# Kernel optimization log

Measured on AMD Instinct MI355X. Metric: run time of the kernel, lower is better.

## Reference

```python
import jax, jax.numpy as jnp
import numpy as np

PD = 3                      # spatial feature dim (z, y, x)
HB = 1024                   # hash base per lattice coordinate
HOFF = 512                  # offset: lattice coords assumed in [-512, 511]
FILL = np.int32(2**31 - 1)  # sentinel for padded hash slots
EPS = 2.220446049250313e-16 # np.finfo('float').eps as in the torch module

def _elev_mat():
    # Embedding onto hyperplane sum(x)=0 with std-dev scale factors
    # (canonical permutohedral-lattice elevation, Adams et al.).
    E = np.zeros((PD + 1, PD), np.float32)
    E[0] = 1.0
    for i in range(1, PD + 1):
        E[i, i - 1] = -i
        E[i, i:] = 1.0
    inv_std = np.sqrt(2.0 / 3.0) * (PD + 1)
    scale = inv_std / np.sqrt(np.arange(1, PD + 1) * np.arange(2, PD + 2))
    return (E * scale[None, :]).astype(np.float32)

_EMAT = _elev_mat()
_IU = np.triu(np.ones((PD + 1, PD + 1), bool), 1)   # j > i
_IL = np.tril(np.ones((PD + 1, PD + 1), bool), -1)  # j < i

def _hash(k):  # (..., PD) int32 -> (...,) int32, injective for |coord| < 512
    return ((k[..., 0] + HOFF) * HB + (k[..., 1] + HOFF)) * HB + (k[..., 2] + HOFF)

def permutohedral(values, features):
    """Splat-blur-slice Gaussian filter. values (N,VD), features (N,PD)."""
    N, VD = values.shape
    elevated = features @ jnp.asarray(_EMAT).T                  # (N, PD+1)
    # nearest remainder-0 lattice point (nearest multiple of PD+1, ties -> down)
    v = elevated / (PD + 1)
    up, down = jnp.ceil(v), jnp.floor(v)
    rem0 = jnp.where(up - v < v - down, up, down) * (PD + 1)
    diff = elevated - rem0
    lt = diff[:, :, None] < diff[:, None, :]
    le = diff[:, :, None] <= diff[:, None, :]
    rank = (lt & _IU).sum(-1) + (le & _IL).sum(-1)              # (N, PD+1) int32
    rank = rank + jnp.round(rem0.sum(-1) / (PD + 1)).astype(rank.dtype)[:, None]
    shift = jnp.where(rank < 0, PD + 1, 0) + jnp.where(rank > PD, -(PD + 1), 0)
    rank = rank + shift
    rem0 = rem0 + shift.astype(rem0.dtype)
    # barycentric coordinates inside the enclosing simplex
    t = (elevated - rem0) / (PD + 1)                            # (N, PD+1)
    ohA = jax.nn.one_hot(PD - rank, PD + 2, dtype=values.dtype)
    ohB = jax.nn.one_hot(PD + 1 - rank, PD + 2, dtype=values.dtype)
    b = (ohA * t[..., None]).sum(1) - (ohB * t[..., None]).sum(1)
    b = b.at[:, 0].add(1.0 + b[:, PD + 1])
    bary = b[:, :PD + 1]                                        # (N, PD+1)
    # keys of the PD+1 simplex vertices (first PD coords; last is implied)
    rem0i = rem0[:, :PD].astype(jnp.int32)
    ranki = rank[:, :PD].astype(jnp.int32)
    r = jnp.arange(PD + 1, dtype=jnp.int32)[None, :, None]
    keys = rem0i[:, None, :] + jnp.where(ranki[:, None, :] >= PD + 1 - r, r - (PD + 1), r)  # (N,PD+1,PD)
    h = _hash(keys).reshape(-1)                                 # (N*(PD+1),)
    M = h.shape[0]
    uh, inv = jnp.unique(h, size=M, fill_value=FILL, return_inverse=True)
    inv = inv.reshape(-1)
    # splat
    contrib = (values[:, None, :] * bary[:, :, None]).reshape(M, VD)
    lat = jax.ops.segment_sum(contrib, inv, num_segments=M)     # (M, VD)
    # decode unique keys from the (invertible) hash
    k2 = uh % HB - HOFF
    tq = uh // HB
    k1 = tq % HB - HOFF
    k0 = tq // HB - HOFF
    ukeys = jnp.stack([k0, k1, k2], -1).astype(jnp.int32)       # (M, PD)
    valid = (uh != FILL)[:, None]
    # blur with [0.5, 1, 0.5] along each of the PD+1 lattice directions
    def lookup(nk, lat_):
        nh = _hash(nk)
        idx = jnp.clip(jnp.searchsorted(uh, nh), 0, M - 1)
        ok = (uh[idx] == nh)[:, None]
        return jnp.where(ok, lat_[idx], 0.0)
    for j in range(PD + 1):
        o = np.ones(PD, np.int32)
        if j < PD:
            o[j] = -PD
        o = jnp.asarray(o)
        lat = jnp.where(valid, lat + 0.5 * (lookup(ukeys + o, lat) + lookup(ukeys - o, lat)), 0.0)
    # slice
    alpha = 1.0 / (1.0 + 2.0 ** (-PD))
    return alpha * jnp.einsum('nr,nrv->nv', bary, lat[inv.reshape(-1, PD + 1)])

def spatial_features(image, v_gamma, sigma_gamma):
    _, d, h, w = image.shape
    z = jnp.arange(d, dtype=jnp.float32)[:, None, None]
    y = jnp.arange(h, dtype=jnp.float32)[None, :, None]
    x = jnp.arange(w, dtype=jnp.float32)[None, None, :]
    zz = v_gamma[0] * jnp.broadcast_to(z, (d, h, w)) / sigma_gamma[0]
    xx = v_gamma[1] * jnp.broadcast_to(x, (d, h, w)) / sigma_gamma[1]
    yy = v_gamma[2] * jnp.broadcast_to(y, (d, h, w)) / sigma_gamma[2]
    return jnp.stack([zz, yy, xx], axis=3)                      # (d,h,w,3)

def setup_inputs() -> dict:
    key = jax.random.key(0)
    k1, k2 = jax.random.split(key)
    C, D, H, W = 4, 64, 128, 128
    return {
        'input_': jax.random.normal(k1, (C, D, H, W), jnp.float32),
        'image': jax.random.normal(k2, (1, D, H, W), jnp.float32),
        'v_gamma': jnp.ones((3,), jnp.float32),       # nn.Parameter init [1,1,1]
        'sigma_gamma': 5.0 * jnp.ones((3,), jnp.float32),
    }

def reference(input_, image, v_gamma, sigma_gamma):
    C, d, h, w = input_.shape
    N = d * h * w
    feats = spatial_features(image, v_gamma, sigma_gamma).reshape(N, PD)
    # filter q and the all-ones normalizer in one pass (linear per channel)
    vals = jnp.concatenate([input_.reshape(C, N).T, jnp.ones((N, 1), jnp.float32)], axis=1)
    out = permutohedral(vals, feats)
    q = out[:, :C].T.reshape(C, d, h, w)
    norm = out[:, C].reshape(1, d, h, w)
    return q * (1.0 / (norm + EPS))
```

## Files before the change

### kernel.cpp

```cpp
#include <hip/hip_runtime.h>


#define DD    64
#define HHH   128
#define WWW   128
#define NPTS  (DD * HHH * WWW)
#define LATN  (1 << 17)
#define SH_BITS 10
#define SHSZ (1 << SH_BITS)

__device__ __forceinline__ int encK(int K0, int K1, int K2) {
    return ((K2 >> 2) << 12) | ((K1 >> 2) << 7) | ((K0 >> 2) << 2) | (K0 & 3);
}

__device__ __forceinline__ void pl_geom(int z, int y, int x,
                                        const float* __restrict__ vg,
                                        const float* __restrict__ sg,
                                        int* didx, float* bout) {
    float f0 = vg[0] * (float)z / sg[0];
    float f1 = vg[2] * (float)y / sg[2];
    float f2 = vg[1] * (float)x / sg[1];

    const float m00 = (float)2.3094010767585034;
    const float m01 = (float)1.3333333333333333;
    const float m02 = (float)0.9428090415820634;
    const float m21 = (float)-2.6666666666666665;
    const float m32 = (float)-2.8284271247461903;

    float e[4];
    e[0] =  m00 * f0 + m01 * f1 + m02 * f2;
    e[1] = -m00 * f0 + m01 * f1 + m02 * f2;
    e[2] =  m21 * f1 + m02 * f2;
    e[3] =  m32 * f2;

    float rem0[4];
    int sumr = 0;
    #pragma unroll
    for (int i = 0; i < 4; ++i) {
        float v = e[i] * 0.25f;
        float up = ceilf(v), dn = floorf(v);
        float rr = ((up - v) < (v - dn)) ? up : dn;
        rem0[i] = rr * 4.0f;
        sumr += (int)rem0[i];
    }
    sumr /= 4;

    float diff[4];
    #pragma unroll
    for (int i = 0; i < 4; ++i) diff[i] = e[i] - rem0[i];
    int rank[4] = {0, 0, 0, 0};
    #pragma unroll
    for (int i = 0; i < 4; ++i)
        #pragma unroll
        for (int j = i + 1; j < 4; ++j) {
            if (diff[i] < diff[j]) rank[i]++; else rank[j]++;
        }

    #pragma unroll
    for (int i = 0; i < 4; ++i) {
        rank[i] += sumr;
        if (rank[i] < 0)      { rank[i] += 4; rem0[i] += 4.0f; }
        else if (rank[i] > 3) { rank[i] -= 4; rem0[i] -= 4.0f; }
    }

    float b[5] = {0.f, 0.f, 0.f, 0.f, 0.f};
    #pragma unroll
    for (int i = 0; i < 4; ++i) {
        float t = (e[i] - rem0[i]) * 0.25f;
        b[3 - rank[i]] += t;
        b[4 - rank[i]] -= t;
    }
    b[0] += 1.0f + b[4];

    int k0 = (int)rem0[0], k1 = (int)rem0[1], k2 = (int)rem0[2];
    #pragma unroll
    for (int r = 0; r < 4; ++r) {
        int o0 = (rank[0] >= 4 - r) ? (r - 4) : r;
        int o1 = (rank[1] >= 4 - r) ? (r - 4) : r;
        int o2 = (rank[2] >= 4 - r) ? (r - 4) : r;
        int K0 = (k0 + o0 + 16) & 127;
        int K1 = (k1 + o1 + 48) & 127;
        int K2 = (k2 + o2 + 88) & 127;
        didx[r] = encK(K0, K1, K2);
        bout[r] = b[r];
    }
}

__device__ __forceinline__ void pl_emit(int key, const float* a,
                                        int* skey, float (*sacc)[5],
                                        float* __restrict__ lat,
                                        unsigned char* __restrict__ exists) {
    unsigned idx = ((unsigned)key * 2654435761u) >> (32 - SH_BITS);
    int probes = 0;
    bool inlds = true;
    for (;;) {
        int cur = skey[idx];
        if (cur == key) break;
        if (cur == -1) {
            cur = atomicCAS(&skey[idx], -1, key);
            if (cur == -1 || cur == key) break;
        }
        idx = (idx + 1) & (SHSZ - 1);
        if (++probes >= SHSZ) { inlds = false; break; }
    }
    if (inlds) {
        #pragma unroll
        for (int c = 0; c < 5; ++c) atomicAdd(&sacc[idx][c], a[c]);
    } else {
        float* L = lat + (size_t)key * 5;
        #pragma unroll
        for (int c = 0; c < 5; ++c) atomicAdd(L + c, a[c]);
        exists[key] = 1;
    }
}

__global__ __launch_bounds__(512, 6)
void pl_splat(const float* __restrict__ vals, const float* __restrict__ vg,
              const float* __restrict__ sg, float* __restrict__ lat,
              unsigned char* __restrict__ exists) {
    __shared__ int   skey[SHSZ];
    __shared__ float sacc[SHSZ][5];
    for (int i = threadIdx.x; i < SHSZ; i += 512) {
        skey[i] = -1;
        #pragma unroll
        for (int c = 0; c < 5; ++c) sacc[i][c] = 0.f;
    }
    __syncthreads();

    int bt = blockIdx.x;
    int lx = threadIdx.x & 15;
    int ly = (threadIdx.x >> 4) & 7;
    int lz = threadIdx.x >> 7;
    int x0 = ((bt & 3) << 5) + (lx << 1);
    int y  = (((bt >> 2) & 15) << 3) + ly;
    int z  = ((bt >> 6) << 2) + lz;
    int n0 = (z << 14) + (y << 7) + x0;

    float2 c0 = *(const float2*)(vals + n0);
    float2 c1 = *(const float2*)(vals + NPTS + n0);
    float2 c2 = *(const float2*)(vals + 2 * NPTS + n0);
    float2 c3 = *(const float2*)(vals + 3 * NPTS + n0);

    int ckey[4];
    float acc[4][5];
    {
        int didx[4]; float b[4];
        pl_geom(z, y, x0, vg, sg, didx, b);
        #pragma unroll
        for (int r = 0; r < 4; ++r) {
            ckey[r] = didx[r];
            float w = b[r];
            acc[r][0] = w * c0.x; acc[r][1] = w * c1.x;
            acc[r][2] = w * c2.x; acc[r][3] = w * c3.x;
            acc[r][4] = w;
        }
    }
    {
        int didx[4]; float b[4];
        pl_geom(z, y, x0 + 1, vg, sg, didx, b);
        #pragma unroll
        for (int r = 0; r < 4; ++r) {
            float w = b[r];
            if (didx[r] == ckey[r]) {
                acc[r][0] += w * c0.y; acc[r][1] += w * c1.y;
                acc[r][2] += w * c2.y; acc[r][3] += w * c3.y;
                acc[r][4] += w;
            } else {
                pl_emit(ckey[r], acc[r], skey, sacc, lat, exists);
                ckey[r] = didx[r];
                acc[r][0] = w * c0.y; acc[r][1] = w * c1.y;
                acc[r][2] = w * c2.y; acc[r][3] = w * c3.y;
                acc[r][4] = w;
            }
        }
    }
    #pragma unroll
    for (int r = 0; r < 4; ++r)
        pl_emit(ckey[r], acc[r], skey, sacc, lat, exists);

    __syncthreads();

    int rot = (blockIdx.x * 131) & (SHSZ - 1);
    for (int ii = threadIdx.x; ii < SHSZ; ii += 512) {
        int i = (ii + rot) & (SHSZ - 1);
        int key = skey[i];
        if (key < 0) continue;
        exists[key] = 1;
        float* L = lat + (size_t)key * 5;
        #pragma unroll
        for (int c = 0; c < 5; ++c) atomicAdd(L + c, sacc[i][c]);
    }
}

__global__ __launch_bounds__(256)
void pl_blur(const float* __restrict__ lin, float* __restrict__ lout,
             const unsigned char* __restrict__ exists,
             int d0, int d1, int d2) {
    int didx = blockIdx.x * 256 + threadIdx.x;
    if (didx >= LATN) return;
    if (!exists[didx]) return;
    int r  = didx & 3;
    int K0 = (((didx >> 2)  & 31) << 2) | r;
    int K1 = (((didx >> 7)  & 31) << 2) | r;
    int K2 = (((didx >> 12) & 31) << 2) | r;
    float acc[5];
    const float* S = lin + (size_t)didx * 5;
    #pragma unroll
    for (int c = 0; c < 5; ++c) acc[c] = S[c];
    #pragma unroll
    for (int sgn = 0; sgn < 2; ++sgn) {
        int a0 = sgn ? -d0 : d0;
        int a1 = sgn ? -d1 : d1;
        int a2 = sgn ? -d2 : d2;
        int P0 = K0 + a0, P1 = K1 + a1, P2 = K2 + a2;
        if (((unsigned)P0 < 128u) & ((unsigned)P1 < 128u) & ((unsigned)P2 < 128u)) {
            const float* L = lin + (size_t)encK(P0, P1, P2) * 5;
            #pragma unroll
            for (int c = 0; c < 5; ++c) acc[c] += 0.5f * L[c];
        }
    }
    float* O = lout + (size_t)didx * 5;
    #pragma unroll
    for (int c = 0; c < 5; ++c) O[c] = acc[c];
}

__global__ __launch_bounds__(256)
void pl_slice(const float* __restrict__ vg, const float* __restrict__ sg,
              const float* __restrict__ lat, float* __restrict__ out) {
    int n = blockIdx.x * 256 + threadIdx.x;
    if (n >= NPTS) return;
    int z = n >> 14;
    int y = (n >> 7) & 127;
    int x = n & 127;
    int didx[4]; float b[4];
    pl_geom(z, y, x, vg, sg, didx, b);
    float a0 = 0.f, a1 = 0.f, a2 = 0.f, a3 = 0.f, a4 = 0.f;
    #pragma unroll
    for (int r = 0; r < 4; ++r) {
        float w = b[r];
        const float* L = lat + (size_t)didx[r] * 5;
        a0 += w * L[0]; a1 += w * L[1]; a2 += w * L[2]; a3 += w * L[3]; a4 += w * L[4];
    }
    const float alpha = (float)(1.0 / 1.125);
    float norm = alpha * a4 + (float)2.220446049250313e-16;
    float invn = 1.0f / norm;
    out[n]            = (alpha * a0) * invn;
    out[NPTS + n]     = (alpha * a1) * invn;
    out[2 * NPTS + n] = (alpha * a2) * invn;
    out[3 * NPTS + n] = (alpha * a3) * invn;
}

extern "C" void kernel_launch(void* const* d_in, const int* in_sizes, int n_in,
                              void* d_out, int out_size, void* d_ws, size_t ws_size,
                              hipStream_t stream) {
    const float* input = (const float*)d_in[0];
    const float* vg = (const float*)d_in[2];
    const float* sg = (const float*)d_in[3];
    float* out = (float*)d_out;

    char* ws = (char*)d_ws;
    size_t off = 0;
    float* lat0 = (float*)(ws + off);            off += (size_t)LATN * 5 * 4;
    float* lat1 = (float*)(ws + off);            off += (size_t)LATN * 5 * 4;
    unsigned char* exists = (unsigned char*)(ws + off); off += LATN;

    hipMemsetAsync(lat0, 0, (size_t)LATN * 5 * 4, stream);
    hipMemsetAsync(lat1, 0, (size_t)LATN * 5 * 4, stream);
    hipMemsetAsync(exists, 0, LATN, stream);

    pl_splat<<<1024, dim3(512), 0, stream>>>(input, vg, sg, lat0, exists);

    const int offs[4][3] = {{-3, 1, 1}, {1, -3, 1}, {1, 1, -3}, {1, 1, 1}};
    float* bufs[2] = {lat0, lat1};
    for (int j = 0; j < 4; ++j) {
        pl_blur<<<LATN / 256, dim3(256), 0, stream>>>(bufs[j & 1], bufs[(j & 1) ^ 1],
                                                      exists,
                                                      offs[j][0], offs[j][1], offs[j][2]);
    }
    pl_slice<<<NPTS / 256, dim3(256), 0, stream>>>(vg, sg, lat0, out);
}
```

Baseline: 186.8 us.

## Fuse blur passes and slice into one persistent kernel with grid barriers

Splat now handles four x-points per thread, so each block covers a larger tile and only half as many blocks launch. Its global atomics are spread across four replicated lattice copies to reduce contention, and those copies are summed inside the first blur pass. The four blur passes and the slice are fused into a single kernel that uses software grid-wide barriers in place of separate launches. Three memsets are merged into one covering a larger region. The grid barrier assumes all 512 blocks are co-resident, which risks deadlock if they are not, and the extra lattice copies increase memset and read traffic.

Result: slower. 537.8 us (+187.9%).

```diff
diff --git a/kernel.cpp b/kernel.cpp
--- a/kernel.cpp
+++ b/kernel.cpp
@@ -6,6 +6,7 @@
 #define WWW   128
 #define NPTS  (DD * HHH * WWW)
 #define LATN  (1 << 17)
+#define LATF  (LATN * 5)
 #define SH_BITS 10
 #define SHSZ (1 << SH_BITS)
 
@@ -88,7 +89,7 @@
 
 __device__ __forceinline__ void pl_emit(int key, const float* a,
                                         int* skey, float (*sacc)[5],
-                                        float* __restrict__ lat,
+                                        float* __restrict__ latc,
                                         unsigned char* __restrict__ exists) {
     unsigned idx = ((unsigned)key * 2654435761u) >> (32 - SH_BITS);
     int probes = 0;
@@ -107,16 +108,16 @@
         #pragma unroll
         for (int c = 0; c < 5; ++c) atomicAdd(&sacc[idx][c], a[c]);
     } else {
-        float* L = lat + (size_t)key * 5;
+        float* L = latc + (size_t)key * 5;
         #pragma unroll
         for (int c = 0; c < 5; ++c) atomicAdd(L + c, a[c]);
         exists[key] = 1;
     }
 }
 
-__global__ __launch_bounds__(512, 6)
+__global__ __launch_bounds__(512, 4)
 void pl_splat(const float* __restrict__ vals, const float* __restrict__ vg,
-              const float* __restrict__ sg, float* __restrict__ lat,
+              const float* __restrict__ sg, float* __restrict__ latc,
               unsigned char* __restrict__ exists) {
     __shared__ int   skey[SHSZ];
     __shared__ float sacc[SHSZ][5];
@@ -127,19 +128,26 @@
     }
     __syncthreads();
 
+    float* mycopy = latc + (size_t)(blockIdx.x & 3) * LATF;
+
     int bt = blockIdx.x;
-    int lx = threadIdx.x & 15;
-    int ly = (threadIdx.x >> 4) & 7;
+    int xs = threadIdx.x & 7;
+    int ly = (threadIdx.x >> 3) & 15;
     int lz = threadIdx.x >> 7;
-    int x0 = ((bt & 3) << 5) + (lx << 1);
-    int y  = (((bt >> 2) & 15) << 3) + ly;
-    int z  = ((bt >> 6) << 2) + lz;
+    int xsl = ((xs & 3) << 1) | (xs >> 2);
+    int x0 = ((bt & 3) << 5) + (xsl << 2);
+    int y  = (((bt >> 2) & 7) << 4) + ly;
+    int z  = ((bt >> 5) << 2) + lz;
     int n0 = (z << 14) + (y << 7) + x0;
 
-    float2 c0 = *(const float2*)(vals + n0);
-    float2 c1 = *(const float2*)(vals + NPTS + n0);
-    float2 c2 = *(const float2*)(vals + 2 * NPTS + n0);
-    float2 c3 = *(const float2*)(vals + 3 * NPTS + n0);
+    float4 q0 = *(const float4*)(vals + n0);
+    float4 q1 = *(const float4*)(vals + NPTS + n0);
+    float4 q2 = *(const float4*)(vals + 2 * NPTS + n0);
+    float4 q3 = *(const float4*)(vals + 3 * NPTS + n0);
+    float ch0[4] = {q0.x, q0.y, q0.z, q0.w};
+    float ch1[4] = {q1.x, q1.y, q1.z, q1.w};
+    float ch2[4] = {q2.x, q2.y, q2.z, q2.w};
+    float ch3[4] = {q3.x, q3.y, q3.z, q3.w};
 
     int ckey[4];
     float acc[4][5];
@@ -150,33 +158,34 @@
         for (int r = 0; r < 4; ++r) {
             ckey[r] = didx[r];
             float w = b[r];
-            acc[r][0] = w * c0.x; acc[r][1] = w * c1.x;
-            acc[r][2] = w * c2.x; acc[r][3] = w * c3.x;
+            acc[r][0] = w * ch0[0]; acc[r][1] = w * ch1[0];
+            acc[r][2] = w * ch2[0]; acc[r][3] = w * ch3[0];
             acc[r][4] = w;
         }
     }
-    {
+    #pragma unroll
+    for (int p = 1; p < 4; ++p) {
         int didx[4]; float b[4];
-        pl_geom(z, y, x0 + 1, vg, sg, didx, b);
+        pl_geom(z, y, x0 + p, vg, sg, didx, b);
         #pragma unroll
         for (int r = 0; r < 4; ++r) {
             float w = b[r];
             if (didx[r] == ckey[r]) {
-                acc[r][0] += w * c0.y; acc[r][1] += w * c1.y;
-                acc[r][2] += w * c2.y; acc[r][3] += w * c3.y;
+                acc[r][0] += w * ch0[p]; acc[r][1] += w * ch1[p];
+                acc[r][2] += w * ch2[p]; acc[r][3] += w * ch3[p];
                 acc[r][4] += w;
             } else {
-                pl_emit(ckey[r], acc[r], skey, sacc, lat, exists);
+                pl_emit(ckey[r], acc[r], skey, sacc, mycopy, exists);
                 ckey[r] = didx[r];
-                acc[r][0] = w * c0.y; acc[r][1] = w * c1.y;
-                acc[r][2] = w * c2.y; acc[r][3] = w * c3.y;
+                acc[r][0] = w * ch0[p]; acc[r][1] = w * ch1[p];
+                acc[r][2] = w * ch2[p]; acc[r][3] = w * ch3[p];
                 acc[r][4] = w;
             }
         }
     }
     #pragma unroll
     for (int r = 0; r < 4; ++r)
-        pl_emit(ckey[r], acc[r], skey, sacc, lat, exists);
+        pl_emit(ckey[r], acc[r], skey, sacc, mycopy, exists);
 
     __syncthreads();
 
@@ -186,68 +195,133 @@
         int key = skey[i];
         if (key < 0) continue;
         exists[key] = 1;
-        float* L = lat + (size_t)key * 5;
+        float* L = mycopy + (size_t)key * 5;
         #pragma unroll
         for (int c = 0; c < 5; ++c) atomicAdd(L + c, sacc[i][c]);
     }
 }
 
+__device__ __forceinline__ void gbar(int* cnt, int nblk) {
+    __syncthreads();
+    __threadfence();
+    if (threadIdx.x == 0) {
+        __hip_atomic_fetch_add(cnt, 1, __ATOMIC_RELEASE, __HIP_MEMORY_SCOPE_AGENT);
+        while (__hip_atomic_load(cnt, __ATOMIC_ACQUIRE, __HIP_MEMORY_SCOPE_AGENT) < nblk)
+            __builtin_amdgcn_s_sleep(2);
+    }
+    __syncthreads();
+    __threadfence();
+}
+
+__device__ __forceinline__ void nbr_add1(const float* __restrict__ in,
+                                         int K0, int K1, int K2, float* a) {
+    if (((unsigned)K0 < 128u) & ((unsigned)K1 < 128u) & ((unsigned)K2 < 128u)) {
+        const float* L = in + (size_t)encK(K0, K1, K2) * 5;
+        #pragma unroll
+        for (int c = 0; c < 5; ++c) a[c] += 0.5f * L[c];
+    }
+}
+__device__ __forceinline__ void nbr_add4(const float* __restrict__ in,
+                                         int K0, int K1, int K2, float* a) {
+    if (((unsigned)K0 < 128u) & ((unsigned)K1 < 128u) & ((unsigned)K2 < 128u)) {
+        size_t o = (size_t)encK(K0, K1, K2) * 5;
+        #pragma unroll
+        for (int c = 0; c < 5; ++c)
+            a[c] += 0.5f * (in[o + c] + in[LATF + o + c] +
+                            in[2 * LATF + o + c] + in[3 * LATF + o + c]);
+    }
+}
+
 __global__ __launch_bounds__(256)
-void pl_blur(const float* __restrict__ lin, float* __restrict__ lout,
-             const unsigned char* __restrict__ exists,
-             int d0, int d1, int d2) {
+void pl_blur_slice(const float* __restrict__ latc, float* __restrict__ A,
+                   float* __restrict__ B, const unsigned char* __restrict__ exists,
+                   int* __restrict__ bar,
+                   const float* __restrict__ vg, const float* __restrict__ sg,
+                   float* __restrict__ out) {
     int didx = blockIdx.x * 256 + threadIdx.x;
-    if (didx >= LATN) return;
-    if (!exists[didx]) return;
     int r  = didx & 3;
     int K0 = (((didx >> 2)  & 31) << 2) | r;
     int K1 = (((didx >> 7)  & 31) << 2) | r;
     int K2 = (((didx >> 12) & 31) << 2) | r;
-    float acc[5];
-    const float* S = lin + (size_t)didx * 5;
-    #pragma unroll
-    for (int c = 0; c < 5; ++c) acc[c] = S[c];
-    #pragma unroll
-    for (int sgn = 0; sgn < 2; ++sgn) {
-        int a0 = sgn ? -d0 : d0;
-        int a1 = sgn ? -d1 : d1;
-        int a2 = sgn ? -d2 : d2;
-        int P0 = K0 + a0, P1 = K1 + a1, P2 = K2 + a2;
-        if (((unsigned)P0 < 128u) & ((unsigned)P1 < 128u) & ((unsigned)P2 < 128u)) {
-            const float* L = lin + (size_t)encK(P0, P1, P2) * 5;
-            #pragma unroll
-            for (int c = 0; c < 5; ++c) acc[c] += 0.5f * L[c];
-        }
-    }
-    float* O = lout + (size_t)didx * 5;
-    #pragma unroll
-    for (int c = 0; c < 5; ++c) O[c] = acc[c];
-}
-
-__global__ __launch_bounds__(256)
-void pl_slice(const float* __restrict__ vg, const float* __restrict__ sg,
-              const float* __restrict__ lat, float* __restrict__ out) {
-    int n = blockIdx.x * 256 + threadIdx.x;
-    if (n >= NPTS) return;
-    int z = n >> 14;
-    int y = (n >> 7) & 127;
-    int x = n & 127;
-    int didx[4]; float b[4];
-    pl_geom(z, y, x, vg, sg, didx, b);
-    float a0 = 0.f, a1 = 0.f, a2 = 0.f, a3 = 0.f, a4 = 0.f;
-    #pragma unroll
-    for (int r = 0; r < 4; ++r) {
-        float w = b[r];
-        const float* L = lat + (size_t)didx[r] * 5;
-        a0 += w * L[0]; a1 += w * L[1]; a2 += w * L[2]; a3 += w * L[3]; a4 += w * L[4];
-    }
-    const float alpha = (float)(1.0 / 1.125);
-    float norm = alpha * a4 + (float)2.220446049250313e-16;
-    float invn = 1.0f / norm;
-    out[n]            = (alpha * a0) * invn;
-    out[NPTS + n]     = (alpha * a1) * invn;
-    out[2 * NPTS + n] = (alpha * a2) * invn;
-    out[3 * NPTS + n] = (alpha * a3) * invn;
+    bool act = exists[didx] != 0;
+    int nblk = gridDim.x;
+
+    if (act) {
+        float a[5];
+        size_t o = (size_t)didx * 5;
+        #pragma unroll
+        for (int c = 0; c < 5; ++c)
+            a[c] = latc[o + c] + latc[LATF + o + c] +
+                   latc[2 * LATF + o + c] + latc[3 * LATF + o + c];
+        nbr_add4(latc, K0 - 3, K1 + 1, K2 + 1, a);
+        nbr_add4(latc, K0 + 3, K1 - 1, K2 - 1, a);
+        float* O = A + o;
+        #pragma unroll
+        for (int c = 0; c < 5; ++c) O[c] = a[c];
+    }
+    gbar(bar + 0, nblk);
+
+    if (act) {
+        float a[5];
+        const float* S = A + (size_t)didx * 5;
+        #pragma unroll
+        for (int c = 0; c < 5; ++c) a[c] = S[c];
+        nbr_add1(A, K0 + 1, K1 - 3, K2 + 1, a);
+        nbr_add1(A, K0 - 1, K1 + 3, K2 - 1, a);
+        float* O = B + (size_t)didx * 5;
+        #pragma unroll
+        for (int c = 0; c < 5; ++c) O[c] = a[c];
+    }
+    gbar(bar + 1, nblk);
+
+    if (act) {
+        float a[5];
+        const float* S = B + (size_t)didx * 5;
+        #pragma unroll
+        for (int c = 0; c < 5; ++c) a[c] = S[c];
+        nbr_add1(B, K0 + 1, K1 + 1, K2 - 3, a);
+        nbr_add1(B, K0 - 1, K1 - 1, K2 + 3, a);
+        float* O = A + (size_t)didx * 5;
+        #pragma unroll
+        for (int c = 0; c < 5; ++c) O[c] = a[c];
+    }
+    gbar(bar + 2, nblk);
+
+    if (act) {
+        float a[5];
+        const float* S = A + (size_t)didx * 5;
+        #pragma unroll
+        for (int c = 0; c < 5; ++c) a[c] = S[c];
+        nbr_add1(A, K0 + 1, K1 + 1, K2 + 1, a);
+        nbr_add1(A, K0 - 1, K1 - 1, K2 - 1, a);
+        float* O = B + (size_t)didx * 5;
+        #pragma unroll
+        for (int c = 0; c < 5; ++c) O[c] = a[c];
+    }
+    gbar(bar + 3, nblk);
+
+    for (int n = blockIdx.x * 256 + threadIdx.x; n < NPTS; n += LATN) {
+        int z = n >> 14;
+        int y = (n >> 7) & 127;
+        int x = n & 127;
+        int didx4[4]; float b[4];
+        pl_geom(z, y, x, vg, sg, didx4, b);
+        float a0 = 0.f, a1 = 0.f, a2 = 0.f, a3 = 0.f, a4 = 0.f;
+        #pragma unroll
+        for (int rr = 0; rr < 4; ++rr) {
+            float w = b[rr];
+            const float* L = B + (size_t)didx4[rr] * 5;
+            a0 += w * L[0]; a1 += w * L[1]; a2 += w * L[2];
+            a3 += w * L[3]; a4 += w * L[4];
+        }
+        const float alpha = (float)(1.0 / 1.125);
+        float norm = alpha * a4 + (float)2.220446049250313e-16;
+        float invn = 1.0f / norm;
+        out[n]            = (alpha * a0) * invn;
+        out[NPTS + n]     = (alpha * a1) * invn;
+        out[2 * NPTS + n] = (alpha * a2) * invn;
+        out[3 * NPTS + n] = (alpha * a3) * invn;
+    }
 }
 
 extern "C" void kernel_launch(void* const* d_in, const int* in_sizes, int n_in,
@@ -259,23 +333,16 @@
     float* out = (float*)d_out;
 
     char* ws = (char*)d_ws;
-    size_t off = 0;
-    float* lat0 = (float*)(ws + off);            off += (size_t)LATN * 5 * 4;
-    float* lat1 = (float*)(ws + off);            off += (size_t)LATN * 5 * 4;
-    unsigned char* exists = (unsigned char*)(ws + off); off += LATN;
-
-    hipMemsetAsync(lat0, 0, (size_t)LATN * 5 * 4, stream);
-    hipMemsetAsync(lat1, 0, (size_t)LATN * 5 * 4, stream);
-    hipMemsetAsync(exists, 0, LATN, stream);
-
-    pl_splat<<<1024, dim3(512), 0, stream>>>(input, vg, sg, lat0, exists);
-
-    const int offs[4][3] = {{-3, 1, 1}, {1, -3, 1}, {1, 1, -3}, {1, 1, 1}};
-    float* bufs[2] = {lat0, lat1};
-    for (int j = 0; j < 4; ++j) {
-        pl_blur<<<LATN / 256, dim3(256), 0, stream>>>(bufs[j & 1], bufs[(j & 1) ^ 1],
-                                                      exists,
-                                                      offs[j][0], offs[j][1], offs[j][2]);
-    }
-    pl_slice<<<NPTS / 256, dim3(256), 0, stream>>>(vg, sg, lat0, out);
-}
+    float* latc = (float*)ws;
+    float* A    = latc + (size_t)4 * LATF;
+    float* B    = A + LATF;
+    unsigned char* exists = (unsigned char*)(B + LATF);
+    int* bar    = (int*)(exists + LATN);
+
+    size_t zbytes = (size_t)6 * LATF * 4 + LATN + 64;
+    hipMemsetAsync(ws, 0, zbytes, stream);
+
+    pl_splat<<<512, dim3(512), 0, stream>>>(input, vg, sg, latc, exists);
+    pl_blur_slice<<<LATN / 256, dim3(256), 0, stream>>>(latc, A, B, exists, bar,
+                                                        vg, sg, out);
+}
```
